# Kernel optimization log

Hardware: AMD Instinct MI355X
Metric: run time of the kernel (lower is better)

Reference implementation:

```python
import jax, jax.numpy as jnp
import numpy as np

N = 20000       # nodes
E = 500000      # edges
D = 256         # dim_in == dim_out (residual requires equality)
T = 4           # num_layers
NTYPES = 3      # cfg.edge_types = [0, 1, 2]
NU = 1          # cfg nu; nu_v2 = False -> delay = max(k - NU, 0) = k - 1


def setup_inputs() -> dict:
    key = jax.random.key(0)
    ks = jax.random.split(key, 8)
    x = jax.random.normal(ks[0], (N, D), dtype=jnp.float32)
    edge_index = jax.random.randint(ks[1], (2, E), 0, N, dtype=jnp.int32)
    hop = jax.random.randint(ks[2], (E,), 1, T + 1, dtype=jnp.int32)   # k in 1..T
    etype = jax.random.randint(ks[3], (E,), 0, NTYPES, dtype=jnp.int32)
    edge_attr = jnp.stack([hop, etype], axis=1)  # [E, 2]
    scale = 0.05
    W_edge = scale * jax.random.normal(ks[4], (T, NTYPES, D, D), dtype=jnp.float32)
    b_edge = scale * jax.random.normal(ks[5], (T, NTYPES, D), dtype=jnp.float32)
    # hop layers W(k, t) for k in 2..t+1; index (t, k-2); max k = T -> T-1 slots
    W_hop = scale * jax.random.normal(ks[6], (T, T - 1, D, D), dtype=jnp.float32)
    b_hop = scale * jax.random.normal(ks[7], (T, T - 1, D), dtype=jnp.float32)
    return {"x": x, "edge_index": edge_index, "edge_attr": edge_attr,
            "W_edge": W_edge, "b_edge": b_edge, "W_hop": W_hop, "b_hop": b_hop}


def _gnn_layer(h_src, src, dst, mask, n_nodes):
    # GNNLayer: linear transform at source nodes then sum-aggregate over the
    # masked edge subset (equivalent to restricting edge_index to that subset).
    msg = jnp.where(mask[:, None], h_src[src], jnp.float32(0.0))  # [E, D]
    return jax.ops.segment_sum(msg, dst, num_segments=n_nodes)    # [N, D]


def reference(x, edge_index, edge_attr, W_edge, b_edge, W_hop, b_hop):
    n_nodes = x.shape[0]
    src, dst = edge_index[0], edge_index[1]
    hop, etype = edge_attr[:, 0], edge_attr[:, 1]
    xs = []
    for t in range(T):
        xs.append(x)
        acc = jnp.zeros_like(x)
        # 1-hop relational layers, one per edge type e
        for e in range(NTYPES):
            h = xs[t] @ W_edge[t, e] + b_edge[t, e]          # transform at node level
            acc = acc + _gnn_layer(h, src, dst, etype == e, n_nodes)
        # delayed multi-hop layers, k = 2..t+1, reading x[t - delay]
        for k in range(2, t + 2):
            delay = max(k - NU, 0)  # nu_v2 = False
            h = xs[t - delay] @ W_hop[t, k - 2] + b_hop[t, k - 2]
            acc = acc + _gnn_layer(h, src, dst, hop == k, n_nodes)
        x = xs[t] + jax.nn.relu(acc)  # residual; cfg.gnn.l2norm = False
    return x
```

## Files before the change

### kernel.cpp

```cpp
#include <hip/hip_runtime.h>


#define NN 20000
#define NROWP 20032
#define NE 500000
#define DD 256
#define TT 4
#define NT 3
#define SCANN (12 * NN)
#define NB12 235

typedef _Float16 f16;
typedef _Float16 f16x8 __attribute__((ext_vector_type(8)));
typedef _Float16 f16x4v __attribute__((ext_vector_type(4)));
typedef float f32x4 __attribute__((ext_vector_type(4)));

__device__ __forceinline__ void gload_lds16(const void* g, void* l) {
  __builtin_amdgcn_global_load_lds(
      (const __attribute__((address_space(1))) unsigned int*)g,
      (__attribute__((address_space(3))) unsigned int*)l, 16, 0, 0);
}


__global__ void k_hist(const int* __restrict__ ei, const int* __restrict__ ea,
                       int* __restrict__ cnt12) {
  int e = blockIdx.x * 256 + threadIdx.x;
  if (e >= NE) return;
  int dst = ei[NE + e];
  int hop = ea[2 * e];
  int et  = ea[2 * e + 1];
  atomicAdd(&cnt12[((dst * 3 + et) << 2) | (hop - 1)], 1);
}


__global__ __launch_bounds__(1024) void k_scan_blk(
    const int* __restrict__ cnt, int* __restrict__ crow, int* __restrict__ bsum) {
  __shared__ int wsum[16];
  int tid = threadIdx.x, lane = tid & 63, wv = tid >> 6;
  int i = blockIdx.x * 1024 + tid;
  int v = (i < SCANN) ? cnt[i] : 0;
  int s = v;
#pragma unroll
  for (int off = 1; off < 64; off <<= 1) {
    int t = __shfl_up(s, off, 64);
    if (lane >= off) s += t;
  }
  if (lane == 63) wsum[wv] = s;
  __syncthreads();
  if (wv == 0) {
    int ws = (lane < 16) ? wsum[lane] : 0;
#pragma unroll
    for (int off = 1; off < 16; off <<= 1) {
      int t = __shfl_up(ws, off, 64);
      if (lane >= off) ws += t;
    }
    if (lane < 16) wsum[lane] = ws;
  }
  __syncthreads();
  int excl = ((wv == 0) ? 0 : wsum[wv - 1]) + s - v;
  if (i < SCANN) crow[i] = excl;
  if (tid == 1023) bsum[blockIdx.x] = wsum[15];
}

__global__ __launch_bounds__(256) void k_scan_top(
    int* __restrict__ bsum, int* __restrict__ crow) {
  __shared__ int wsum2[4];
  int tid = threadIdx.x, lane = tid & 63, wv = tid >> 6;
  int v = (tid < NB12) ? bsum[tid] : 0;
  int s = v;
#pragma unroll
  for (int off = 1; off < 64; off <<= 1) {
    int t = __shfl_up(s, off, 64);
    if (lane >= off) s += t;
  }
  if (lane == 63) wsum2[wv] = s;
  __syncthreads();
  int add = 0;
#pragma unroll
  for (int w = 0; w < 4; w++) add += (w < wv) ? wsum2[w] : 0;
  int excl = add + s - v;
  if (tid < NB12) bsum[tid] = excl;
  if (tid == NB12 - 1) crow[SCANN] = excl + v;
}

__global__ __launch_bounds__(1024) void k_scan_fix(
    int* __restrict__ crow, int* __restrict__ ccur, const int* __restrict__ bsum) {
  int i = blockIdx.x * 1024 + threadIdx.x;
  if (i >= SCANN) return;
  int val = crow[i] + bsum[blockIdx.x];
  crow[i] = val;
  ccur[i] = val;
}

__global__ void k_scatter(const int* __restrict__ ei, const int* __restrict__ ea,
                          int* __restrict__ ccur, int* __restrict__ crec) {
  int e = blockIdx.x * 256 + threadIdx.x;
  if (e >= NE) return;
  int src = ei[e];
  int dst = ei[NE + e];
  int hop = ea[2 * e];
  int et  = ea[2 * e + 1];
  int pos = atomicAdd(&ccur[((dst * 3 + et) << 2) | (hop - 1)], 1);
  crec[pos] = src;
}


__global__ __launch_bounds__(256) void k_cnt6(
    const int* __restrict__ crow12, int* __restrict__ cnt) {
  int v = blockIdx.x * 256 + threadIdx.x;
  if (v >= NN) return;
  int h2 = 0, h3 = 0, h4 = 0;
#pragma unroll
  for (int et = 0; et < 3; et++) {
    int base = (v * 3 + et) * 4;
    int b0 = crow12[base], b1 = crow12[base + 1], b2 = crow12[base + 2],
        b3 = crow12[base + 3], b4 = crow12[base + 4];
    cnt[et * NN + v] = b4 - b0;
    h2 += b2 - b1;
    h3 += b3 - b2;
    h4 += b4 - b3;
  }
  cnt[3 * NN + v] = h2;
  cnt[4 * NN + v] = h3;
  cnt[5 * NN + v] = h4;
}


__global__ __launch_bounds__(256) void k_wsplit(
    const float* __restrict__ W_edge, const float* __restrict__ W_hop,
    f16* __restrict__ Wout) {
  __shared__ float tile[64][65];
  int w = blockIdx.z;
  int tk = blockIdx.x * 64;
  int tn = blockIdx.y * 64;
  const float* src = (w < 12) ? (W_edge + (size_t)w * 65536)
                              : (W_hop + (size_t)(w - 12) * 65536);
  f16* dst = Wout + (size_t)w * 65536;
  int c = threadIdx.x & 63;
  int r0 = threadIdx.x >> 6;
#pragma unroll
  for (int i = 0; i < 16; i++) {
    int r = i * 4 + r0;
    tile[r][c] = src[(size_t)(tk + r) * 256 + tn + c] * 16.0f;
  }
  __syncthreads();
#pragma unroll
  for (int i = 0; i < 16; i++) {
    int r = i * 4 + r0;
    dst[(size_t)(tn + r) * 256 + tk + c] = (f16)tile[c][r];
  }
}


__global__ void k_xcast(const float* __restrict__ x, f16* __restrict__ xh) {
  size_t i = (size_t)(blockIdx.x * 256 + threadIdx.x) * 4;
  float4 v = *(const float4*)(x + i);
  f16x4v h = { (f16)v.x, (f16)v.y, (f16)v.z, (f16)v.w };
  *(f16x4v*)(xh + i) = h;
}


struct AggArgs {
  f16* out[6];
};

#define GSEG(LO, HI, DOH, ACCH)                                         \
  {                                                                     \
    int e_ = (LO);                                                      \
    for (; e_ + 4 <= (HI); e_ += 4) {                                   \
      int s0_ = crec[e_ + half], s1_ = crec[e_ + 2 + half];             \
      f16x8 h0_ = *(const f16x8*)(xb + (size_t)s0_ * 512);              \
      f16x8 h1_ = *(const f16x8*)(xb + (size_t)s1_ * 512);              \
      float tb_[8];                                                     \
      _Pragma("unroll") for (int j = 0; j < 8; j++) {                   \
        tb_[j] = (float)h0_[j] + (float)h1_[j];                         \
        aE[j] += tb_[j];                                                \
      }                                                                 \
      if (DOH) {                                                        \
        _Pragma("unroll") for (int j = 0; j < 8; j++) ACCH[j] += tb_[j];\
      }                                                                 \
    }                                                                   \
    if (e_ + 2 <= (HI)) {                                               \
      int s0_ = crec[e_ + half];                                        \
      f16x8 h0_ = *(const f16x8*)(xb + (size_t)s0_ * 512);              \
      float tb_[8];                                                     \
      _Pragma("unroll") for (int j = 0; j < 8; j++) {                   \
        tb_[j] = (float)h0_[j];                                         \
        aE[j] += tb_[j];                                                \
      }                                                                 \
      if (DOH) {                                                        \
        _Pragma("unroll") for (int j = 0; j < 8; j++) ACCH[j] += tb_[j];\
      }                                                                 \
      e_ += 2;                                                          \
    }                                                                   \
    if (e_ < (HI) && half == 0) {                                       \
      int s0_ = crec[e_];                                               \
      f16x8 h0_ = *(const f16x8*)(xb + (size_t)s0_ * 512);              \
      float tb_[8];                                                     \
      _Pragma("unroll") for (int j = 0; j < 8; j++) {                   \
        tb_[j] = (float)h0_[j];                                         \
        aE[j] += tb_[j];                                                \
      }                                                                 \
      if (DOH) {                                                        \
        _Pragma("unroll") for (int j = 0; j < 8; j++) ACCH[j] += tb_[j];\
      }                                                                 \
    }                                                                   \
  }

__global__ __launch_bounds__(256) void k_aggregate(
    const f16* __restrict__ xh,
    const int* __restrict__ crow12,
    const int* __restrict__ crec,
    AggArgs args)
{
  int wave = threadIdx.x >> 6;
  int lane = threadIdx.x & 63;
  int half = lane >> 5;
  int chunk = lane & 31;
  int v = blockIdx.x * 4 + wave;
  const char* xb = (const char*)xh + chunk * 16;
  const bool doH2 = (args.out[3] != nullptr);
  const bool doH3 = (args.out[4] != nullptr);
  const bool doH4 = (args.out[5] != nullptr);
  const float s = 0.015625f;

  float aH2[8], aH3[8], aH4[8];
#pragma unroll
  for (int j = 0; j < 8; j++) { aH2[j] = 0.f; aH3[j] = 0.f; aH4[j] = 0.f; }

#pragma unroll
  for (int et = 0; et < 3; et++) {
    int base = (v * 3 + et) * 4;
    int b0 = crow12[base], b1 = crow12[base + 1], b2 = crow12[base + 2],
        b3 = crow12[base + 3], b4 = crow12[base + 4];
    float aE[8];
#pragma unroll
    for (int j = 0; j < 8; j++) aE[j] = 0.f;
    GSEG(b0, b1, false, aH2);
    GSEG(b1, b2, doH2, aH2);
    GSEG(b2, b3, doH3, aH3);
    GSEG(b3, b4, doH4, aH4);
#pragma unroll
    for (int j = 0; j < 8; j++) aE[j] += __shfl_xor(aE[j], 32, 64);
    if (half == 0) {
      f16x8 o;
#pragma unroll
      for (int j = 0; j < 8; j++) o[j] = (f16)(aE[j] * s);
      *(f16x8*)((char*)args.out[et] + (size_t)v * 512 + chunk * 16) = o;
    }
  }

  if (doH2) {
#pragma unroll
    for (int j = 0; j < 8; j++) aH2[j] += __shfl_xor(aH2[j], 32, 64);
    if (half == 0) {
      f16x8 o;
#pragma unroll
      for (int j = 0; j < 8; j++) o[j] = (f16)(aH2[j] * s);
      *(f16x8*)((char*)args.out[3] + (size_t)v * 512 + chunk * 16) = o;
    }
  }
  if (doH3) {
#pragma unroll
    for (int j = 0; j < 8; j++) aH3[j] += __shfl_xor(aH3[j], 32, 64);
    if (half == 0) {
      f16x8 o;
#pragma unroll
      for (int j = 0; j < 8; j++) o[j] = (f16)(aH3[j] * s);
      *(f16x8*)((char*)args.out[4] + (size_t)v * 512 + chunk * 16) = o;
    }
  }
  if (doH4) {
#pragma unroll
    for (int j = 0; j < 8; j++) aH4[j] += __shfl_xor(aH4[j], 32, 64);
    if (half == 0) {
      f16x8 o;
#pragma unroll
      for (int j = 0; j < 8; j++) o[j] = (f16)(aH4[j] * s);
      *(f16x8*)((char*)args.out[5] + (size_t)v * 512 + chunk * 16) = o;
    }
  }
}


struct GemmArgs {
  const f16* A[6];
  const f16* W[6];
  const float* bias[6];
  const int*   cnt[6];
  int nch;
  int write_f32;
  const f16* xh_in;
  f16*       xh_out;
  float*     f32_out;
};

__global__ __launch_bounds__(512) void k_gemm(GemmArgs args) {
  __shared__ __align__(16) f16 sA[2][4096];
  __shared__ __align__(16) f16 sB[2][8192];
  const int tid = threadIdx.x;
  const int lane = tid & 63;
  const int wave = tid >> 6;
  const int wm = (wave >> 2) * 32;
  const int wn = (wave & 3) * 32;

  const int orig = blockIdx.x;
  const int xcd = orig & 7, idx = orig >> 3;
  const int wg = (xcd < 2 ? xcd * 79 : 158 + (xcd - 2) * 78) + idx;
  const int m0 = (wg >> 1) * 64;
  const int n0 = (wg & 1) * 128;
  const int nch = args.nch;
  const int Titer = nch * 4;

  f32x4 acc[2][2];
#pragma unroll
  for (int mi = 0; mi < 2; mi++)
#pragma unroll
    for (int ni = 0; ni < 2; ni++) acc[mi][ni] = (f32x4){0.f, 0.f, 0.f, 0.f};

  int srcA, ldsAoffU;
  {
    int s = tid;
    int ks = s >> 8, r = (s >> 2) & 63, pc = s & 3;
    int lc = pc ^ ((r >> 1) & 3);
    srcA = r * 512 + ks * 64 + lc * 16;
    ldsAoffU = wave * 1024;
  }
  int srcB[2], ldsBoffU[2];
#pragma unroll
  for (int i = 0; i < 2; i++) {
    int s = i * 512 + tid;
    int ks = s >> 9, r = (s >> 2) & 127, pc = s & 3;
    int lc = pc ^ ((r >> 1) & 3);
    srcB[i] = r * 512 + ks * 64 + lc * 16;
    ldsBoffU[i] = i * 8192 + wave * 1024;
  }

  const int fr = lane & 15;
  const int gq = lane >> 4;
  int offA[2][2], offB[2][2];
#pragma unroll
  for (int mi = 0; mi < 2; mi++) {
    int rr = wm + mi * 16 + fr;
    int swz = (gq ^ ((rr >> 1) & 3)) << 4;
#pragma unroll
    for (int ks = 0; ks < 2; ks++) offA[mi][ks] = ks * 4096 + rr * 64 + swz;
  }
#pragma unroll
  for (int ni = 0; ni < 2; ni++) {
    int rr = wn + ni * 16 + fr;
    int swz = (gq ^ ((rr >> 1) & 3)) << 4;
#pragma unroll
    for (int ks = 0; ks < 2; ks++) offB[ni][ks] = ks * 8192 + rr * 64 + swz;
  }

  auto stage = [&](int buf, int j) {
    int c = j >> 2, kb = (j & 3) * 128;
    const char* pa = (const char*)args.A[c] + (size_t)m0 * 512 + kb;
    const char* pb = (const char*)args.W[c] + (size_t)n0 * 512 + kb;
    gload_lds16(pa + srcA, (char*)sA[buf] + ldsAoffU);
#pragma unroll
    for (int i = 0; i < 2; i++)
      gload_lds16(pb + srcB[i], (char*)sB[buf] + ldsBoffU[i]);
  };

  stage(0, 0);
  stage(1, 1);

  for (int j = 0; j < Titer; ++j) {
    const int p = j & 1;
    if (j + 1 < Titer) {
      asm volatile("s_waitcnt vmcnt(3)" ::: "memory");
    } else {
      asm volatile("s_waitcnt vmcnt(0)" ::: "memory");
    }
    __builtin_amdgcn_s_barrier();
    __builtin_amdgcn_sched_barrier(0);
    {
      f16x8 fA[2][2], fB[2][2];
#pragma unroll
      for (int ks = 0; ks < 2; ks++) {
#pragma unroll
        for (int mi = 0; mi < 2; mi++)
          fA[ks][mi] = *(const f16x8*)((const char*)sA[p] + offA[mi][ks]);
#pragma unroll
        for (int ni = 0; ni < 2; ni++)
          fB[ks][ni] = *(const f16x8*)((const char*)sB[p] + offB[ni][ks]);
      }
#pragma unroll
      for (int ks = 0; ks < 2; ks++)
#pragma unroll
        for (int mi = 0; mi < 2; mi++)
#pragma unroll
          for (int ni = 0; ni < 2; ni++)
            acc[mi][ni] = __builtin_amdgcn_mfma_f32_16x16x32_f16(
                fA[ks][mi], fB[ks][ni], acc[mi][ni], 0, 0, 0);
    }
    __builtin_amdgcn_s_barrier();
    __builtin_amdgcn_sched_barrier(0);
    if (j + 2 < Titer) stage(p, j + 2);
  }

  float bcol[2][6];
#pragma unroll
  for (int ni = 0; ni < 2; ni++) {
    int gcol = n0 + wn + ni * 16 + fr;
#pragma unroll
    for (int c = 0; c < 6; c++)
      bcol[ni][c] = (c < nch) ? args.bias[c][gcol] : 0.f;
  }
  const int rowq = gq * 4;
#pragma unroll
  for (int mi = 0; mi < 2; mi++) {
#pragma unroll
    for (int rI = 0; rI < 4; rI++) {
      int grow = m0 + wm + mi * 16 + rowq + rI;
      if (grow < NN) {
        float cv[6];
#pragma unroll
        for (int c = 0; c < 6; c++)
          cv[c] = (c < nch) ? (float)args.cnt[c][grow] : 0.f;
        size_t rowoff = (size_t)grow * DD;
#pragma unroll
        for (int ni = 0; ni < 2; ni++) {
          int gcol = n0 + wn + ni * 16 + fr;
          float v = acc[mi][ni][rI] * 4.0f;
#pragma unroll
          for (int c = 0; c < 6; c++) v += cv[c] * bcol[ni][c];
          float outv = (float)args.xh_in[rowoff + gcol] + fmaxf(v, 0.f);
          args.xh_out[rowoff + gcol] = (f16)outv;
          if (args.write_f32) args.f32_out[rowoff + gcol] = outv;
        }
      }
    }
  }
}


extern "C" void kernel_launch(void* const* d_in, const int* in_sizes, int n_in,
                              void* d_out, int out_size, void* d_ws, size_t ws_size,
                              hipStream_t stream) {
  const float* x      = (const float*)d_in[0];
  const int* edge_index = (const int*)d_in[1];
  const int* edge_attr  = (const int*)d_in[2];
  const float* W_edge = (const float*)d_in[3];
  const float* b_edge = (const float*)d_in[4];
  const float* W_hop  = (const float*)d_in[5];
  const float* b_hop  = (const float*)d_in[6];
  float* out = (float*)d_out;

  char* ws = (char*)d_ws;
  int* cnt    = (int*)ws;
  int* crow12 = cnt + 6 * NN;
  int* ccur12 = crow12 + SCANN + 1;
  int* bsum   = ccur12 + SCANN;
  int* crec   = bsum + NB12;
  size_t int_count = (size_t)6 * NN + (SCANN + 1) + SCANN + NB12 + (size_t)NE;
  const size_t ND  = (size_t)NN * DD;
  const size_t NDP = (size_t)NROWP * DD;
  f16* Wsplit = (f16*)(ws + ((int_count * 4 + 255) & ~(size_t)255));
  f16* xh = Wsplit + (size_t)24 * 65536;
  f16* aggBase = xh + ND;
  f16* agg[9];
  for (int i = 0; i < 9; i++) agg[i] = aggBase + (size_t)i * NDP;
  f16** Cb = agg + 3;

  hipMemsetAsync(ccur12, 0, SCANN * sizeof(int), stream);

  k_hist<<<(NE + 255) / 256, 256, 0, stream>>>(edge_index, edge_attr, ccur12);
  k_scan_blk<<<NB12, 1024, 0, stream>>>(ccur12, crow12, bsum);
  k_scan_top<<<1, 256, 0, stream>>>(bsum, crow12);
  k_scan_fix<<<NB12, 1024, 0, stream>>>(crow12, ccur12, bsum);
  k_scatter<<<(NE + 255) / 256, 256, 0, stream>>>(edge_index, edge_attr, ccur12, crec);
  k_cnt6<<<(NN + 255) / 256, 256, 0, stream>>>(crow12, cnt);
  k_wsplit<<<dim3(4, 4, 24), 256, 0, stream>>>(W_edge, W_hop, Wsplit);
  k_xcast<<<ND / 1024, 256, 0, stream>>>(x, xh);

  for (int t = 0; t < TT; ++t) {
    AggArgs aa{};
    aa.out[0] = agg[0];
    aa.out[1] = agg[1];
    aa.out[2] = agg[2];
    aa.out[3] = (t <= 2) ? Cb[t]     : nullptr;
    aa.out[4] = (t <= 1) ? Cb[3 + t] : nullptr;
    aa.out[5] = (t == 0) ? Cb[5]     : nullptr;
    k_aggregate<<<dim3(NN / 4), 256, 0, stream>>>(xh, crow12, crec, aa);

    GemmArgs ga{};
    for (int e = 0; e < NT; ++e) {
      ga.A[e]    = agg[e];
      ga.W[e]    = Wsplit + (size_t)(t * NT + e) * 65536;
      ga.bias[e] = b_edge + (size_t)(t * NT + e) * DD;
      ga.cnt[e]  = cnt + (size_t)e * NN;
    }
    int nc = NT;
    for (int k = 2; k <= t + 1; ++k) {
      int s = t + 1 - k;
      ga.A[nc]    = (k == 2) ? Cb[s] : (k == 3) ? Cb[3 + s] : Cb[5];
      ga.W[nc]    = Wsplit + (size_t)(12 + t * 3 + (k - 2)) * 65536;
      ga.bias[nc] = b_hop + (size_t)(t * (TT - 1) + (k - 2)) * DD;
      ga.cnt[nc]  = cnt + (size_t)(3 + (k - 2)) * NN;
      nc++;
    }
    for (int c = nc; c < 6; ++c) {
      ga.A[c] = ga.A[0]; ga.W[c] = ga.W[0]; ga.bias[c] = ga.bias[0]; ga.cnt[c] = ga.cnt[0];
    }
    ga.nch = nc;
    ga.write_f32 = (t == TT - 1) ? 1 : 0;
    ga.xh_in  = xh;
    ga.xh_out = xh;
    ga.f32_out = out;
    k_gemm<<<dim3(626), 512, 0, stream>>>(ga);
  }
}
```

Baseline: 469.8 us.

## Split aggregation by feature slice with XCD-aware block mapping

The gather-aggregate kernel now gives each wave a 128-byte feature slice of one node instead of the full 512-byte row. Each 8-lane group handles one of eight edges per step, and a shuffle tree reduces the partial sums. Blocks are remapped so that each XCD pair only touches one quarter of the feature columns, shrinking the per-XCD L2 working set of the gathered fp16 features. The cost is four times as many blocks, repeated reads of the CSR offsets and edge lists, and masked lanes on ragged edge tails.

```diff
diff --git a/kernel.cpp b/kernel.cpp
--- a/kernel.cpp
+++ b/kernel.cpp
@@ -164,49 +164,6 @@
   f16* out[6];
 };
 
-#define GSEG(LO, HI, DOH, ACCH)                                         \
-  {                                                                     \
-    int e_ = (LO);                                                      \
-    for (; e_ + 4 <= (HI); e_ += 4) {                                   \
-      int s0_ = crec[e_ + half], s1_ = crec[e_ + 2 + half];             \
-      f16x8 h0_ = *(const f16x8*)(xb + (size_t)s0_ * 512);              \
-      f16x8 h1_ = *(const f16x8*)(xb + (size_t)s1_ * 512);              \
-      float tb_[8];                                                     \
-      _Pragma("unroll") for (int j = 0; j < 8; j++) {                   \
-        tb_[j] = (float)h0_[j] + (float)h1_[j];                         \
-        aE[j] += tb_[j];                                                \
-      }                                                                 \
-      if (DOH) {                                                        \
-        _Pragma("unroll") for (int j = 0; j < 8; j++) ACCH[j] += tb_[j];\
-      }                                                                 \
-    }                                                                   \
-    if (e_ + 2 <= (HI)) {                                               \
-      int s0_ = crec[e_ + half];                                        \
-      f16x8 h0_ = *(const f16x8*)(xb + (size_t)s0_ * 512);              \
-      float tb_[8];                                                     \
-      _Pragma("unroll") for (int j = 0; j < 8; j++) {                   \
-        tb_[j] = (float)h0_[j];                                         \
-        aE[j] += tb_[j];                                                \
-      }                                                                 \
-      if (DOH) {                                                        \
-        _Pragma("unroll") for (int j = 0; j < 8; j++) ACCH[j] += tb_[j];\
-      }                                                                 \
-      e_ += 2;                                                          \
-    }                                                                   \
-    if (e_ < (HI) && half == 0) {                                       \
-      int s0_ = crec[e_];                                               \
-      f16x8 h0_ = *(const f16x8*)(xb + (size_t)s0_ * 512);              \
-      float tb_[8];                                                     \
-      _Pragma("unroll") for (int j = 0; j < 8; j++) {                   \
-        tb_[j] = (float)h0_[j];                                         \
-        aE[j] += tb_[j];                                                \
-      }                                                                 \
-      if (DOH) {                                                        \
-        _Pragma("unroll") for (int j = 0; j < 8; j++) ACCH[j] += tb_[j];\
-      }                                                                 \
-    }                                                                   \
-  }
-
 __global__ __launch_bounds__(256) void k_aggregate(
     const f16* __restrict__ xh,
     const int* __restrict__ crow12,
@@ -215,14 +172,19 @@
 {
   int wave = threadIdx.x >> 6;
   int lane = threadIdx.x & 63;
-  int half = lane >> 5;
-  int chunk = lane & 31;
-  int v = blockIdx.x * 4 + wave;
-  const char* xb = (const char*)xh + chunk * 16;
+  int rg = lane >> 3;
+  int cc = lane & 7;
+  int orig = blockIdx.x;
+  int xcd = orig & 7;
+  int slice = xcd >> 1;
+  int idx = ((orig >> 3) << 1) + (xcd & 1);
+  int v = idx * 4 + wave;
+  const char* xb = (const char*)xh + slice * 128 + cc * 16;
   const bool doH2 = (args.out[3] != nullptr);
   const bool doH3 = (args.out[4] != nullptr);
   const bool doH4 = (args.out[5] != nullptr);
   const float s = 0.015625f;
+  const size_t outOff = (size_t)v * 512 + slice * 128 + cc * 16;
 
   float aH2[8], aH3[8], aH4[8];
 #pragma unroll
@@ -236,48 +198,90 @@
     float aE[8];
 #pragma unroll
     for (int j = 0; j < 8; j++) aE[j] = 0.f;
-    GSEG(b0, b1, false, aH2);
-    GSEG(b1, b2, doH2, aH2);
-    GSEG(b2, b3, doH3, aH3);
-    GSEG(b3, b4, doH4, aH4);
-#pragma unroll
-    for (int j = 0; j < 8; j++) aE[j] += __shfl_xor(aE[j], 32, 64);
-    if (half == 0) {
+
+    for (int e = b0; e < b4; e += 8) {
+      int i = e + rg;
+      int il = (i < b4) ? i : (b4 - 1);
+      int src = crec[il];
+      f16x8 h = *(const f16x8*)(xb + (size_t)src * 512);
+      float fv = (i < b4) ? 1.f : 0.f;
+      float r[8];
+#pragma unroll
+      for (int j = 0; j < 8; j++) {
+        r[j] = (float)h[j] * fv;
+        aE[j] += r[j];
+      }
+      if (doH2) {
+        float f = (i >= b1 && i < b2) ? 1.f : 0.f;
+#pragma unroll
+        for (int j = 0; j < 8; j++) aH2[j] += r[j] * f;
+      }
+      if (doH3) {
+        float f = (i >= b2 && i < b3) ? 1.f : 0.f;
+#pragma unroll
+        for (int j = 0; j < 8; j++) aH3[j] += r[j] * f;
+      }
+      if (doH4) {
+        float f = (i >= b3 && i < b4) ? 1.f : 0.f;
+#pragma unroll
+        for (int j = 0; j < 8; j++) aH4[j] += r[j] * f;
+      }
+    }
+
+#pragma unroll
+    for (int j = 0; j < 8; j++) {
+      aE[j] += __shfl_xor(aE[j], 8, 64);
+      aE[j] += __shfl_xor(aE[j], 16, 64);
+      aE[j] += __shfl_xor(aE[j], 32, 64);
+    }
+    if (rg == 0) {
       f16x8 o;
 #pragma unroll
       for (int j = 0; j < 8; j++) o[j] = (f16)(aE[j] * s);
-      *(f16x8*)((char*)args.out[et] + (size_t)v * 512 + chunk * 16) = o;
+      *(f16x8*)((char*)args.out[et] + outOff) = o;
     }
   }
 
   if (doH2) {
 #pragma unroll
-    for (int j = 0; j < 8; j++) aH2[j] += __shfl_xor(aH2[j], 32, 64);
-    if (half == 0) {
+    for (int j = 0; j < 8; j++) {
+      aH2[j] += __shfl_xor(aH2[j], 8, 64);
+      aH2[j] += __shfl_xor(aH2[j], 16, 64);
+      aH2[j] += __shfl_xor(aH2[j], 32, 64);
+    }
+    if (rg == 0) {
       f16x8 o;
 #pragma unroll
       for (int j = 0; j < 8; j++) o[j] = (f16)(aH2[j] * s);
-      *(f16x8*)((char*)args.out[3] + (size_t)v * 512 + chunk * 16) = o;
+      *(f16x8*)((char*)args.out[3] + outOff) = o;
     }
   }
   if (doH3) {
 #pragma unroll
-    for (int j = 0; j < 8; j++) aH3[j] += __shfl_xor(aH3[j], 32, 64);
-    if (half == 0) {
+    for (int j = 0; j < 8; j++) {
+      aH3[j] += __shfl_xor(aH3[j], 8, 64);
+      aH3[j] += __shfl_xor(aH3[j], 16, 64);
+      aH3[j] += __shfl_xor(aH3[j], 32, 64);
+    }
+    if (rg == 0) {
       f16x8 o;
 #pragma unroll
       for (int j = 0; j < 8; j++) o[j] = (f16)(aH3[j] * s);
-      *(f16x8*)((char*)args.out[4] + (size_t)v * 512 + chunk * 16) = o;
+      *(f16x8*)((char*)args.out[4] + outOff) = o;
     }
   }
   if (doH4) {
 #pragma unroll
-    for (int j = 0; j < 8; j++) aH4[j] += __shfl_xor(aH4[j], 32, 64);
-    if (half == 0) {
+    for (int j = 0; j < 8; j++) {
+      aH4[j] += __shfl_xor(aH4[j], 8, 64);
+      aH4[j] += __shfl_xor(aH4[j], 16, 64);
+      aH4[j] += __shfl_xor(aH4[j], 32, 64);
+    }
+    if (rg == 0) {
       f16x8 o;
 #pragma unroll
       for (int j = 0; j < 8; j++) o[j] = (f16)(aH4[j] * s);
-      *(f16x8*)((char*)args.out[5] + (size_t)v * 512 + chunk * 16) = o;
+      *(f16x8*)((char*)args.out[5] + outOff) = o;
     }
   }
 }
@@ -484,7 +488,7 @@
     aa.out[3] = (t <= 2) ? Cb[t]     : nullptr;
     aa.out[4] = (t <= 1) ? Cb[3 + t] : nullptr;
     aa.out[5] = (t == 0) ? Cb[5]     : nullptr;
-    k_aggregate<<<dim3(NN / 4), 256, 0, stream>>>(xh, crow12, crec, aa);
+    k_aggregate<<<dim3(NN), 256, 0, stream>>>(xh, crow12, crec, aa);
 
     GemmArgs ga{};
     for (int e = 0; e < NT; ++e) {
```

After: 663.5 us. +41.2%, slower.
